# Kernel optimization log

Hardware: AMD Instinct MI355X
Metric: run time of the kernel (lower is better)

The kernel has to match this reference:

```python
import jax, jax.numpy as jnp
import numpy as np

IN_F = 2
DIM_H = 64
DT = 0.02          # step_size
INTENSITY = 40.0   # Poisson rate multiplier
RATE = jnp.array([10.0, 1.0], dtype=jnp.float32)  # Gamma rates per feature


def _xavier(key, fan_in, fan_out):
    lim = float(np.sqrt(6.0 / (fan_in + fan_out)))
    return jax.random.uniform(key, (fan_in, fan_out), minval=-lim, maxval=lim, dtype=jnp.float32)


def setup_inputs() -> dict:
    key = jax.random.key(0)
    k0, k1, k2 = jax.random.split(key, 3)
    Nsim, steps = 100000, 200
    z0 = jax.random.normal(k0, (Nsim, IN_F), dtype=jnp.float32)
    W1 = _xavier(k1, IN_F, DIM_H)
    b1 = jnp.zeros((DIM_H,), dtype=jnp.float32)
    W2 = _xavier(k2, DIM_H, IN_F)
    b2 = jnp.zeros((IN_F,), dtype=jnp.float32)
    diffusion = jnp.float32(1.0)
    return {"z0": z0, "W1": W1, "b1": b1, "W2": W2, "b2": b2,
            "diffusion": diffusion, "Nsim": Nsim, "steps": steps}


def _drift(x, W1, b1, W2, b2):
    # MLP: Linear(2,64) -> tanh -> Linear(64,2)
    h = jnp.tanh(x @ W1 + b1)
    return h @ W2 + b2


def reference(z0, W1, b1, W2, b2, diffusion, Nsim, steps):
    sqrt_dt = jnp.float32(np.sqrt(DT))
    n = z0.shape[0]

    def step(state, key):
        kp, kn, kg = jax.random.split(key, 3)
        # Poisson(intensity*dt) jump counts, shape [N,1]
        pois = jax.random.poisson(kp, INTENSITY * DT, (n, 1)).astype(jnp.float32)
        a = jnp.broadcast_to(pois, (n, IN_F))  # Gamma concentration per feature
        # Gamma(conc=pois, rate=RATE); conc==0 -> sample is exactly 0
        g = jax.random.gamma(kg, jnp.maximum(a, 1.0), dtype=jnp.float32) / RATE
        jump = jnp.where(a > 0, g, 0.0)
        noise = jax.random.normal(kn, (n, IN_F), dtype=jnp.float32)
        new_state = (state
                     + _drift(state, W1, b1, W2, b2) * DT
                     + diffusion * sqrt_dt * noise
                     + jump)
        return new_state, new_state

    keys = jax.random.split(jax.random.key(42), steps)
    _, path = jax.lax.scan(step, z0, keys)            # [steps, N, F]
    path = jnp.concatenate([z0[None], path], axis=0)   # [steps+1, N, F]
    return jnp.transpose(path, (1, 0, 2))              # [N, steps+1, F]
```

## Files before the change

kernel.cpp:

```cpp
#include <hip/hip_runtime.h>
#include <cstdint>
#include <cmath>

#define DEVINL __device__ __forceinline__

struct U2 { uint32_t a, b; };
typedef float v2f __attribute__((ext_vector_type(2)));

DEVINL uint32_t rotl32(uint32_t x, uint32_t r){ return (x << r) | (x >> (32u - r)); }

DEVINL U2 tf(uint32_t k0, uint32_t k1, uint32_t x0, uint32_t x1){
  const uint32_t k2 = k0 ^ k1 ^ 0x1BD11BDAu;
  x0 += k0; x1 += k1;
#define TFR(r) { x0 += x1; x1 = rotl32(x1,(r)); x1 ^= x0; }
  TFR(13) TFR(15) TFR(26) TFR(6)  x0 += k1; x1 += k2 + 1u;
  TFR(17) TFR(29) TFR(16) TFR(24) x0 += k2; x1 += k0 + 2u;
  TFR(13) TFR(15) TFR(26) TFR(6)  x0 += k0; x1 += k1 + 3u;
  TFR(17) TFR(29) TFR(16) TFR(24) x0 += k1; x1 += k2 + 4u;
  TFR(13) TFR(15) TFR(26) TFR(6)  x0 += k2; x1 += k0 + 5u;
#undef TFR
  U2 r; r.a = x0; r.b = x1; return r;
}

DEVINL uint32_t pbits(uint32_t k0, uint32_t k1, uint32_t idx){
  U2 r = tf(k0, k1, 0u, idx);
  return r.a ^ r.b;
}

DEVINL float u01(uint32_t bits){
  return __uint_as_float((bits >> 9) | 0x3F800000u) - 1.0f;
}

DEVINL float xla_logf(float xin){
  float xf = fmaxf(__uint_as_float(0x00800000u), xin);
  uint32_t ib = __float_as_uint(xf);
  float e = (float)((int)(ib >> 23) - 126);
  float x = __uint_as_float((ib & 0x807fffffu) | 0x3f000000u);
  bool m = x < 0.707106781186547524f;
  float t = m ? x : 0.0f;
  x = __fsub_rn(x, 1.0f);
  if (m) e = __fsub_rn(e, 1.0f);
  x = __fadd_rn(x, t);
  float z = __fmul_rn(x, x);
  float y = 7.0376836292e-2f;
  y = fmaf(y, x, -1.1514610310e-1f);
  y = fmaf(y, x,  1.1676998740e-1f);
  y = fmaf(y, x, -1.2420140846e-1f);
  y = fmaf(y, x,  1.4249322787e-1f);
  y = fmaf(y, x, -1.6668057665e-1f);
  y = fmaf(y, x,  2.0000714765e-1f);
  y = fmaf(y, x, -2.4999993993e-1f);
  y = fmaf(y, x,  3.3333331174e-1f);
  y = __fmul_rn(y, x);
  y = __fmul_rn(y, z);
  y = fmaf(e, -2.12194440e-4f, y);
  y = fmaf(z, -0.5f, y);
  x = __fadd_rn(x, y);
  x = fmaf(e, 0.693359375f, x);
  if (xin == 0.0f) x = __uint_as_float(0xff800000u);
  return x;
}

DEVINL float xla_log1pf(float v){
  float av = fabsf(v);
  if (av < 1e-4f) return __fmul_rn(__fadd_rn(__fmul_rn(-0.5f, v), 1.0f), v);
  return xla_logf(__fadd_rn(v, 1.0f));
}

DEVINL float erfinv32(float x){
  float xx = __fmul_rn(x, x);
  float w = -xla_log1pf(-xx);
  float p;
  if (w < 5.0f){
    float ww = __fsub_rn(w, 2.5f);
    p = 2.81022636e-08f;
    p = __fadd_rn( 3.43273939e-07f, __fmul_rn(p, ww));
    p = __fadd_rn(-3.5233877e-06f,  __fmul_rn(p, ww));
    p = __fadd_rn(-4.39150654e-06f, __fmul_rn(p, ww));
    p = __fadd_rn( 0.00021858087f,  __fmul_rn(p, ww));
    p = __fadd_rn(-0.00125372503f,  __fmul_rn(p, ww));
    p = __fadd_rn(-0.00417768164f,  __fmul_rn(p, ww));
    p = __fadd_rn( 0.246640727f,    __fmul_rn(p, ww));
    p = __fadd_rn( 1.50140941f,     __fmul_rn(p, ww));
  } else {
    float ww = __fsub_rn(sqrtf(w), 3.0f);
    p = -0.000200214257f;
    p = __fadd_rn( 0.000100950558f, __fmul_rn(p, ww));
    p = __fadd_rn( 0.00134934322f,  __fmul_rn(p, ww));
    p = __fadd_rn(-0.00367342844f,  __fmul_rn(p, ww));
    p = __fadd_rn( 0.00573950773f,  __fmul_rn(p, ww));
    p = __fadd_rn(-0.0076224613f,   __fmul_rn(p, ww));
    p = __fadd_rn( 0.00943887047f,  __fmul_rn(p, ww));
    p = __fadd_rn( 1.00167406f,     __fmul_rn(p, ww));
    p = __fadd_rn( 2.83297682f,     __fmul_rn(p, ww));
  }
  return __fmul_rn(p, x);
}

#define SQRT2F (__uint_as_float(0x3FB504F3u))
#define NLOF   (__uint_as_float(0xBF7FFFFFu))

DEVINL float normal_from_bits(uint32_t bits){
  float ff = u01(bits);
  float u = __fadd_rn(__fmul_rn(ff, 2.0f), NLOF);
  u = fmaxf(NLOF, u);
  return __fmul_rn(SQRT2F, erfinv32(u));
}

DEVINL float fast_tanh(float x){
  float ax = fabsf(x);
  float e = __expf(-2.0f * ax);
  float r = (1.0f - e) * __builtin_amdgcn_rcpf(1.0f + e);
  return __builtin_copysignf(r, x);
}

DEVINL v2f f2fma(v2f a, v2f b, v2f c){ return __builtin_elementwise_fma(a, b, c); }

DEVINL float gamma_one(uint32_t gk0, uint32_t gk1, float alpha){
  const float d = __fsub_rn(alpha, (1.0f/3.0f));
  const float c = (1.0f/3.0f) / sqrtf(d);
  U2 K = tf(gk0, gk1, 0u, 0u);
  for (;;) {
    U2 xk = tf(K.a, K.b, 0u, 1u);
    U2 Uk = tf(K.a, K.b, 0u, 2u);
    float xx, v;
    for (;;) {
      U2 sub = tf(xk.a, xk.b, 0u, 1u);
      uint32_t nb = pbits(sub.a, sub.b, 0u);
      xx = normal_from_bits(nb);
      v = __fadd_rn(1.0f, __fmul_rn(xx, c));
      if (v > 0.0f) break;
      xk = tf(xk.a, xk.b, 0u, 0u);
    }
    float X = __fmul_rn(xx, xx);
    float V = __fmul_rn(__fmul_rn(v, v), v);
    float U = u01(pbits(Uk.a, Uk.b, 0u));
    float sq = __fsub_rn(1.0f, __fmul_rn(0.0331f, __fmul_rn(X, X)));
    if (U < sq) return __fmul_rn(d, V);
    float lnU = xla_logf(U);
    float lnV = xla_logf(V);
    float rhs = __fadd_rn(__fmul_rn(X, 0.5f),
                          __fmul_rn(d, __fadd_rn(__fsub_rn(1.0f, V), lnV)));
    if (lnU < rhs) return __fmul_rn(d, V);
    K = tf(K.a, K.b, 0u, 0u);
  }
}

#define NPK 24
#define WSTRIDE (4 + 2*NPK)
#define KEYOFF 8
#define JOFF   16384

__global__ void setup_kernel(uint32_t* __restrict__ ws, int steps){
  int t = blockIdx.x * blockDim.x + threadIdx.x;
  if (t >= steps) return;
  U2 kt = tf(0u, 42u, 0u, (uint32_t)t);
  U2 kp = tf(kt.a, kt.b, 0u, 0u);
  U2 kn = tf(kt.a, kt.b, 0u, 1u);
  U2 kg = tf(kt.a, kt.b, 0u, 2u);
  uint32_t* p = ws + KEYOFF + (size_t)t * WSTRIDE;
  p[0] = kn.a; p[1] = kn.b;
  p[2] = kg.a; p[3] = kg.b;
  uint32_t r0 = kp.a, r1 = kp.b;
  for (int i = 0; i < NPK; ++i) {
    U2 sub = tf(r0, r1, 0u, 1u);
    U2 rn  = tf(r0, r1, 0u, 0u);
    p[4 + 2*i] = sub.a; p[5 + 2*i] = sub.b;
    r0 = rn.a; r1 = rn.b;
  }
}

__global__ __launch_bounds__(256) void pois_kernel(
    uint32_t* __restrict__ ws, int N, int steps, uint32_t POFF, uint32_t COFF)
{
  __shared__ uint32_t cnts[4];
  int e = blockIdx.x * 256 + threadIdx.x;
  int t = blockIdx.y;
  bool act = e < N;
  const uint32_t* __restrict__ p = ws + KEYOFF + (size_t)t * WSTRIDE;
  int pois = 0;
  if (act) {
    float lp = 0.0f; int k = 0;
    #pragma unroll 1
    for (int i = 0; i < NPK; ++i) {
      if (!(lp > -0.8f)) break;
      k++;
      uint32_t bits = pbits(p[4 + 2*i], p[5 + 2*i], (uint32_t)e);
      lp = __fadd_rn(lp, xla_logf(u01(bits)));
    }
    pois = k - 1;
    float* jarr = (float*)(ws + JOFF);
    size_t jb = (size_t)t * (size_t)(2*N) + 2u*(uint32_t)e;
    jarr[jb] = 0.0f; jarr[jb + 1] = 0.0f;
    ((uint8_t*)ws)[(size_t)POFF*4u + (size_t)t*(size_t)N + (size_t)e] = (uint8_t)pois;
  }
  uint64_t b = __ballot(act && (pois > 0));
  int lane = threadIdx.x & 63, w = threadIdx.x >> 6;
  if (lane == 0) cnts[w] = (uint32_t)__popcll(b);
  __syncthreads();
  if (threadIdx.x == 0)
    ws[COFF + (size_t)blockIdx.y * gridDim.x + blockIdx.x] =
        cnts[0] + cnts[1] + cnts[2] + cnts[3];
}

__global__ __launch_bounds__(256) void prefix_kernel(
    uint32_t* __restrict__ ws, uint32_t COFF, uint32_t BOFF, int NB)
{
  __shared__ uint32_t ssum[256];
  int i = threadIdx.x;
  int chunk = (NB + 255) >> 8;
  int lo = i * chunk, hi = lo + chunk; if (hi > NB) hi = NB;
  uint32_t s = 0;
  for (int j = lo; j < hi; ++j) s += ws[COFF + j];
  ssum[i] = s;
  __syncthreads();
  if (i == 0) {
    uint32_t run = 0;
    for (int k = 0; k < 256; ++k) { uint32_t c = ssum[k]; ssum[k] = run; run += c; }
    ws[0] = run;
  }
  __syncthreads();
  uint32_t base = ssum[i];
  for (int j = lo; j < hi; ++j) { ws[BOFF + j] = base; base += ws[COFF + j]; }
}

__global__ __launch_bounds__(256) void scatter_kernel(
    uint32_t* __restrict__ ws, int N, int steps,
    uint32_t POFF, uint32_t BOFF, uint32_t WOFF, uint32_t CAP)
{
  __shared__ uint32_t cnts[4];
  int e = blockIdx.x * 256 + threadIdx.x;
  int t = blockIdx.y;
  bool act = e < N;
  uint32_t pv = 0;
  if (act) pv = ((const uint8_t*)ws)[(size_t)POFF*4u + (size_t)t*(size_t)N + (size_t)e];
  uint64_t b = __ballot(pv > 0);
  int lane = threadIdx.x & 63, w = threadIdx.x >> 6;
  if (lane == 0) cnts[w] = (uint32_t)__popcll(b);
  __syncthreads();
  uint32_t bid = (uint32_t)blockIdx.y * gridDim.x + blockIdx.x;
  uint32_t wb = ws[BOFF + bid];
  for (int w2 = 0; w2 < w; ++w2) wb += cnts[w2];
  if (pv > 0) {
    uint32_t rank = (uint32_t)__popcll(b & ((1ull << lane) - 1ull));
    uint32_t idx = wb + rank;
    if (idx < CAP)
      ws[WOFF + idx] = ((uint32_t)t << 23) | ((uint32_t)e << 6) | pv;
  }
}

__global__ __launch_bounds__(256) void gamma_kernel(
    uint32_t* __restrict__ ws, int N, uint32_t WOFF, uint32_t CAP)
{
  uint32_t total = ws[0]; if (total > CAP) total = CAP;
  uint32_t j = blockIdx.x * 256u + threadIdx.x;
  if (j >= 2u * total) return;
  uint32_t ent = ws[WOFF + (j >> 1)];
  uint32_t t = ent >> 23, e = (ent >> 6) & 0x1FFFFu, pv = ent & 0x3Fu;
  const uint32_t* __restrict__ p = ws + KEYOFF + (size_t)t * WSTRIDE;
  uint32_t f = j & 1u;
  U2 gk = tf(p[2], p[3], 0u, 2u*e + f);
  float s = gamma_one(gk.a, gk.b, (float)pv);
  float* jarr = (float*)(ws + JOFF);
  jarr[(size_t)t * (size_t)(2*N) + (size_t)(2u*e + f)] = f ? s : (s / 10.0f);
}

__global__ __launch_bounds__(256) void jump_kernel(
    uint32_t* __restrict__ ws, int N, int steps)
{
  int e = blockIdx.x * 256 + threadIdx.x;
  int t = blockIdx.y;
  if (e >= N) return;
  const uint32_t* __restrict__ p = ws + KEYOFF + (size_t)t * WSTRIDE;
  const uint32_t ue = (uint32_t)e;
  float lp = 0.0f; int k = 0;
  #pragma unroll 1
  for (int i = 0; i < NPK; ++i) {
    if (!(lp > -0.8f)) break;
    k++;
    uint32_t bits = pbits(p[4 + 2*i], p[5 + 2*i], ue);
    lp = __fadd_rn(lp, xla_logf(u01(bits)));
  }
  int pois = k - 1;
  float* jarr = (float*)(ws + JOFF);
  size_t jbase = (size_t)t * (size_t)(2*N) + (size_t)(2*e);
  float j0 = 0.0f, j1 = 0.0f;
  if (pois > 0) {
    uint32_t kg0 = p[2], kg1 = p[3];
    float alpha = (float)pois;
    U2 gk0 = tf(kg0, kg1, 0u, 2u*ue);
    j0 = gamma_one(gk0.a, gk0.b, alpha) / 10.0f;
    U2 gk1 = tf(kg0, kg1, 0u, 2u*ue + 1u);
    j1 = gamma_one(gk1.a, gk1.b, alpha);
  }
  jarr[jbase] = j0; jarr[jbase + 1] = j1;
}

#define IBLK 256
__global__ __launch_bounds__(IBLK) void integrate_kernel(
    const float* __restrict__ z0, const float* __restrict__ W1,
    const float* __restrict__ b1, const float* __restrict__ W2,
    const float* __restrict__ b2, const float* __restrict__ diffp,
    const uint32_t* __restrict__ ws, float* __restrict__ out,
    int N, int steps)
{
  __shared__ float smem[322];
  for (int k = threadIdx.x; k < 322; k += IBLK) {
    float v;
    if (k < 128)      v = W1[k];
    else if (k < 192) v = b1[k - 128];
    else if (k < 320) v = W2[k - 192];
    else              v = b2[k - 320];
    smem[k] = v;
  }
  __syncthreads();
  const float* sW1 = smem;
  const float* sb1 = smem + 128;
  const float* sW2 = smem + 192;
  const float* sb2 = smem + 320;

  int tid = blockIdx.x * IBLK + threadIdx.x;
  if (tid >= 2 * N) return;
  const int e = tid >> 1;
  const int f = tid & 1;
  const uint32_t utid = (uint32_t)tid;

  float x = z0[tid];
  const size_t obase = (size_t)e * (size_t)(steps + 1) * 2u + (size_t)f;
  out[obase] = x;

  const float DTf  = 0.02f;
  const float sqdt = (float)0.14142135623730951;
  const float coef = __fmul_rn(diffp[0], sqdt);
  const int   hbase = f << 5;
  const float* __restrict__ jarr = (const float*)(ws + JOFF);

  for (int t = 0; t < steps; ++t) {
    const uint32_t* __restrict__ p = ws + KEYOFF + (size_t)t * WSTRIDE;

    float jump = jarr[(size_t)t * (size_t)(2*N) + utid];

    float nf = normal_from_bits(pbits(p[0], p[1], utid));

    float xo = __shfl_xor(x, 1, 64);
    float xf0 = (f == 0) ? x : xo;
    float xf1 = (f == 0) ? xo : x;
    v2f xv0 = (v2f){xf0, xf0};
    v2f xv1 = (v2f){xf1, xf1};
    v2f acc = (v2f){0.0f, 0.0f};
    #pragma unroll
    for (int j = 0; j < 16; ++j) {
      int h = hbase + 2*j;
      v2f w1lo = *(const v2f*)&sW1[h];
      v2f w1hi = *(const v2f*)&sW1[64 + h];
      v2f b1v  = *(const v2f*)&sb1[h];
      v2f pre  = f2fma(xv0, w1lo, f2fma(xv1, w1hi, b1v));
      float hv0 = fast_tanh(pre.x);
      float hv1 = fast_tanh(pre.y);
      v2f w2a = *(const v2f*)&sW2[2*h];
      v2f w2b = *(const v2f*)&sW2[2*h + 2];
      acc = f2fma((v2f){hv0, hv0}, w2a, acc);
      acc = f2fma((v2f){hv1, hv1}, w2b, acc);
    }
    float q0 = acc.x + __shfl_xor(acc.x, 1, 64);
    float q1 = acc.y + __shfl_xor(acc.y, 1, 64);
    float dr = sb2[f] + ((f == 0) ? q0 : q1);

    x = __fadd_rn(__fadd_rn(__fadd_rn(x, __fmul_rn(dr, DTf)),
                            __fmul_rn(coef, nf)), jump);
    out[obase + (size_t)(t + 1) * 2u] = x;
  }
}

__global__ __launch_bounds__(64) void sim_fallback_kernel(
    const float* __restrict__ z0, const float* __restrict__ W1,
    const float* __restrict__ b1, const float* __restrict__ W2,
    const float* __restrict__ b2, const float* __restrict__ diffp,
    const uint32_t* __restrict__ ws, float* __restrict__ out,
    int N, int steps)
{
  __shared__ float smem[322];
  for (int k = threadIdx.x; k < 322; k += 64) {
    float v;
    if (k < 128)      v = W1[k];
    else if (k < 192) v = b1[k - 128];
    else if (k < 320) v = W2[k - 192];
    else              v = b2[k - 320];
    smem[k] = v;
  }
  __syncthreads();
  const float* sW1 = smem;
  const float* sb1 = smem + 128;
  const float* sW2 = smem + 192;
  const float* sb2 = smem + 320;

  int tid = blockIdx.x * 64 + threadIdx.x;
  if (tid >= 2 * N) return;
  const int e = tid >> 1;
  const int f = tid & 1;
  const uint32_t ue   = (uint32_t)e;
  const uint32_t utid = (uint32_t)tid;

  float x = z0[tid];
  const size_t obase = (size_t)e * (size_t)(steps + 1) * 2u + (size_t)f;
  out[obase] = x;

  const float DTf  = 0.02f;
  const float sqdt = (float)0.14142135623730951;
  const float coef = __fmul_rn(diffp[0], sqdt);
  const int   hbase = f << 5;

  for (int t = 0; t < steps; ++t) {
    const uint32_t* __restrict__ p = ws + KEYOFF + (size_t)t * WSTRIDE;
    int pois;
    {
      float lp = 0.0f;
      pois = NPK - 1;
      #pragma unroll 1
      for (int m = 0; m < NPK/2; ++m) {
        int i0 = 2*m + f;
        uint32_t bits = pbits(p[4 + 2*i0], p[5 + 2*i0], ue);
        float lmine = xla_logf(u01(bits));
        float lother = __shfl_xor(lmine, 1, 64);
        float la = (f == 0) ? lmine : lother;
        float lb = (f == 0) ? lother : lmine;
        float s1 = __fadd_rn(lp, la);
        float s2 = __fadd_rn(s1, lb);
        if (!(s1 > -0.8f)) { pois = 2*m; break; }
        if (!(s2 > -0.8f)) { pois = 2*m + 1; break; }
        lp = s2;
      }
    }
    float nf = normal_from_bits(pbits(p[0], p[1], utid));
    float jump = 0.0f;
    if (pois > 0) {
      U2 gk = tf(p[2], p[3], 0u, utid);
      float s = gamma_one(gk.a, gk.b, (float)pois);
      jump = (f == 0) ? (s / 10.0f) : s;
    }
    float xo = __shfl_xor(x, 1, 64);
    float xf0 = (f == 0) ? x : xo;
    float xf1 = (f == 0) ? xo : x;
    float p0 = 0.0f, p1 = 0.0f;
    #pragma unroll
    for (int i = 0; i < 32; ++i) {
      int h = hbase + i;
      float hv = fast_tanh(fmaf(xf0, sW1[h], fmaf(xf1, sW1[64 + h], sb1[h])));
      p0 = fmaf(hv, sW2[2*h],     p0);
      p1 = fmaf(hv, sW2[2*h + 1], p1);
    }
    float q0 = p0 + __shfl_xor(p0, 1, 64);
    float q1 = p1 + __shfl_xor(p1, 1, 64);
    float dr = sb2[f] + ((f == 0) ? q0 : q1);
    x = __fadd_rn(__fadd_rn(__fadd_rn(x, __fmul_rn(dr, DTf)),
                            __fmul_rn(coef, nf)), jump);
    out[obase + (size_t)(t + 1) * 2u] = x;
  }
}

extern "C" void kernel_launch(void* const* d_in, const int* in_sizes, int n_in,
                              void* d_out, int out_size, void* d_ws, size_t ws_size,
                              hipStream_t stream) {
  const float* z0  = (const float*)d_in[0];
  const float* W1  = (const float*)d_in[1];
  const float* b1  = (const float*)d_in[2];
  const float* W2  = (const float*)d_in[3];
  const float* b2  = (const float*)d_in[4];
  const float* dif = (const float*)d_in[5];
  int N = in_sizes[0] / 2;
  int steps = out_size / (N * 2) - 1;
  uint32_t* ws = (uint32_t*)d_ws;
  int total = 2 * N;

  hipLaunchKernelGGL(setup_kernel, dim3((steps + 255) / 256), dim3(256), 0, stream,
                     ws, steps);

  size_t JSZ = (size_t)2 * (size_t)N * (size_t)steps;
  size_t PSZ = ((size_t)N * (size_t)steps + 3u) / 4u;
  int    NBX = (N + 255) / 256;
  size_t NB  = (size_t)NBX * (size_t)steps;
  size_t CAP = ((size_t)N * (size_t)steps * 11u) / 16u;
  size_t POFFs = (size_t)JOFF + JSZ;
  size_t COFFs = POFFs + PSZ;
  size_t BOFFs = COFFs + NB;
  size_t WOFFs = BOFFs + NB;
  size_t need0 = (WOFFs + CAP) * 4u;
  size_t need1 = ((size_t)JOFF + JSZ) * 4u;
  bool pk = (N < (1 << 17)) && (steps < (1 << 9)) && (steps <= 314) &&
            (WOFFs + CAP < 0xFFFFFFFFull);

  if (pk && ws_size >= need0) {
    hipLaunchKernelGGL(pois_kernel, dim3(NBX, steps), dim3(256), 0, stream,
                       ws, N, steps, (uint32_t)POFFs, (uint32_t)COFFs);
    hipLaunchKernelGGL(prefix_kernel, dim3(1), dim3(256), 0, stream,
                       ws, (uint32_t)COFFs, (uint32_t)BOFFs, (int)NB);
    hipLaunchKernelGGL(scatter_kernel, dim3(NBX, steps), dim3(256), 0, stream,
                       ws, N, steps, (uint32_t)POFFs, (uint32_t)BOFFs,
                       (uint32_t)WOFFs, (uint32_t)CAP);
    size_t gth = 2u * CAP;
    hipLaunchKernelGGL(gamma_kernel, dim3((gth + 255) / 256), dim3(256), 0, stream,
                       ws, N, (uint32_t)WOFFs, (uint32_t)CAP);
    hipLaunchKernelGGL(integrate_kernel, dim3((total + IBLK - 1) / IBLK), dim3(IBLK),
                       0, stream, z0, W1, b1, W2, b2, dif, ws, (float*)d_out, N, steps);
  } else if (steps <= 314 && ws_size >= need1) {
    hipLaunchKernelGGL(jump_kernel, dim3((N + 255) / 256, steps), dim3(256), 0, stream,
                       ws, N, steps);
    hipLaunchKernelGGL(integrate_kernel, dim3((total + IBLK - 1) / IBLK), dim3(IBLK),
                       0, stream, z0, W1, b1, W2, b2, dif, ws, (float*)d_out, N, steps);
  } else {
    hipLaunchKernelGGL(sim_fallback_kernel, dim3((total + 63) / 64), dim3(64), 0, stream,
                       z0, W1, b1, W2, b2, dif, ws, (float*)d_out, N, steps);
  }
}
```

Measured before the change: 1.664 ms.

## Compact Poisson sampling across elements per wave and scalarize MLP drift loop

The Poisson kernel now launches 64-thread blocks where each lane handles four elements in sequence. A lane that finishes one element's Poisson loop moves on to the next immediately, so lanes with short draws no longer sit idle waiting for the longest draw in the wave. The per-block count is reduced with a wave shuffle instead of shared memory and a syncthreads. Separately, the integrate kernel's hidden-layer loop is rewritten from packed v2f FMAs to scalar fmaf, which may change the instruction mix. The block count per step is still 256 elements, so the count layout the later kernels rely on is unchanged.

```diff
diff --git a/kernel.cpp b/kernel.cpp
--- a/kernel.cpp
+++ b/kernel.cpp
@@ -5,7 +5,6 @@
 #define DEVINL __device__ __forceinline__
 
 struct U2 { uint32_t a, b; };
-typedef float v2f __attribute__((ext_vector_type(2)));
 
 DEVINL uint32_t rotl32(uint32_t x, uint32_t r){ return (x << r) | (x >> (32u - r)); }
 
@@ -114,8 +113,6 @@
   return __builtin_copysignf(r, x);
 }
 
-DEVINL v2f f2fma(v2f a, v2f b, v2f c){ return __builtin_elementwise_fma(a, b, c); }
-
 DEVINL float gamma_one(uint32_t gk0, uint32_t gk1, float alpha){
   const float d = __fsub_rn(alpha, (1.0f/3.0f));
   const float c = (1.0f/3.0f) / sqrtf(d);
@@ -170,37 +167,63 @@
   }
 }
 
-__global__ __launch_bounds__(256) void pois_kernel(
+#define PEL 4
+__global__ __launch_bounds__(64) void pois_kernel(
     uint32_t* __restrict__ ws, int N, int steps, uint32_t POFF, uint32_t COFF)
 {
-  __shared__ uint32_t cnts[4];
-  int e = blockIdx.x * 256 + threadIdx.x;
-  int t = blockIdx.y;
-  bool act = e < N;
+  const int lane = threadIdx.x;
+  const int t = blockIdx.y;
+  const int base = blockIdx.x * (64 * PEL);
   const uint32_t* __restrict__ p = ws + KEYOFF + (size_t)t * WSTRIDE;
-  int pois = 0;
-  if (act) {
-    float lp = 0.0f; int k = 0;
-    #pragma unroll 1
-    for (int i = 0; i < NPK; ++i) {
-      if (!(lp > -0.8f)) break;
+
+  int poisv[PEL];
+  #pragma unroll
+  for (int j = 0; j < PEL; ++j) poisv[j] = -1;
+
+  int cur = 0;
+  int e = base + lane;
+  float lp = 0.0f; int k = 0;
+  bool done = (e >= N);
+
+  #pragma unroll 1
+  for (int guard = 0; guard < PEL * NPK + PEL + 1; ++guard) {
+    if (!__any(!done)) break;
+    if (!done) {
+      if (!(lp > -0.8f)) {
+        poisv[cur] = k - 1;
+        cur++;
+        lp = 0.0f; k = 0;
+        int ne = base + cur * 64 + lane;
+        if (cur >= PEL || ne >= N) done = true;
+        else e = ne;
+      }
+    }
+    if (!done) {
+      uint32_t bits = pbits(p[4 + 2*k], p[5 + 2*k], (uint32_t)e);
+      lp = __fadd_rn(lp, xla_logf(u01(bits)));
       k++;
-      uint32_t bits = pbits(p[4 + 2*i], p[5 + 2*i], (uint32_t)e);
-      lp = __fadd_rn(lp, xla_logf(u01(bits)));
-    }
-    pois = k - 1;
-    float* jarr = (float*)(ws + JOFF);
-    size_t jb = (size_t)t * (size_t)(2*N) + 2u*(uint32_t)e;
-    jarr[jb] = 0.0f; jarr[jb + 1] = 0.0f;
-    ((uint8_t*)ws)[(size_t)POFF*4u + (size_t)t*(size_t)N + (size_t)e] = (uint8_t)pois;
-  }
-  uint64_t b = __ballot(act && (pois > 0));
-  int lane = threadIdx.x & 63, w = threadIdx.x >> 6;
-  if (lane == 0) cnts[w] = (uint32_t)__popcll(b);
-  __syncthreads();
-  if (threadIdx.x == 0)
-    ws[COFF + (size_t)blockIdx.y * gridDim.x + blockIdx.x] =
-        cnts[0] + cnts[1] + cnts[2] + cnts[3];
+      if (k >= NPK) lp = -1.0f;
+    }
+  }
+
+  float* jarr = (float*)(ws + JOFF);
+  uint8_t* pb = (uint8_t*)ws + (size_t)POFF * 4u + (size_t)t * (size_t)N;
+  int mycnt = 0;
+  #pragma unroll
+  for (int j = 0; j < PEL; ++j) {
+    int ej = base + j * 64 + lane;
+    if (ej < N) {
+      pb[ej] = (uint8_t)poisv[j];
+      size_t jb = (size_t)t * (size_t)(2*N) + 2u * (uint32_t)ej;
+      jarr[jb] = 0.0f; jarr[jb + 1] = 0.0f;
+      if (poisv[j] > 0) mycnt++;
+    }
+  }
+  int c = mycnt;
+  #pragma unroll
+  for (int off = 32; off > 0; off >>= 1) c += __shfl_xor(c, off, 64);
+  if (lane == 0)
+    ws[COFF + (size_t)t * gridDim.x + blockIdx.x] = (uint32_t)c;
 }
 
 __global__ __launch_bounds__(256) void prefix_kernel(
@@ -345,25 +368,16 @@
     float xo = __shfl_xor(x, 1, 64);
     float xf0 = (f == 0) ? x : xo;
     float xf1 = (f == 0) ? xo : x;
-    v2f xv0 = (v2f){xf0, xf0};
-    v2f xv1 = (v2f){xf1, xf1};
-    v2f acc = (v2f){0.0f, 0.0f};
+    float p0 = 0.0f, p1 = 0.0f;
     #pragma unroll
-    for (int j = 0; j < 16; ++j) {
-      int h = hbase + 2*j;
-      v2f w1lo = *(const v2f*)&sW1[h];
-      v2f w1hi = *(const v2f*)&sW1[64 + h];
-      v2f b1v  = *(const v2f*)&sb1[h];
-      v2f pre  = f2fma(xv0, w1lo, f2fma(xv1, w1hi, b1v));
-      float hv0 = fast_tanh(pre.x);
-      float hv1 = fast_tanh(pre.y);
-      v2f w2a = *(const v2f*)&sW2[2*h];
-      v2f w2b = *(const v2f*)&sW2[2*h + 2];
-      acc = f2fma((v2f){hv0, hv0}, w2a, acc);
-      acc = f2fma((v2f){hv1, hv1}, w2b, acc);
-    }
-    float q0 = acc.x + __shfl_xor(acc.x, 1, 64);
-    float q1 = acc.y + __shfl_xor(acc.y, 1, 64);
+    for (int i = 0; i < 32; ++i) {
+      int h = hbase + i;
+      float hv = fast_tanh(fmaf(xf0, sW1[h], fmaf(xf1, sW1[64 + h], sb1[h])));
+      p0 = fmaf(hv, sW2[2*h],     p0);
+      p1 = fmaf(hv, sW2[2*h + 1], p1);
+    }
+    float q0 = p0 + __shfl_xor(p0, 1, 64);
+    float q1 = p1 + __shfl_xor(p1, 1, 64);
     float dr = sb2[f] + ((f == 0) ? q0 : q1);
 
     x = __fadd_rn(__fadd_rn(__fadd_rn(x, __fmul_rn(dr, DTf)),
@@ -490,7 +504,7 @@
             (WOFFs + CAP < 0xFFFFFFFFull);
 
   if (pk && ws_size >= need0) {
-    hipLaunchKernelGGL(pois_kernel, dim3(NBX, steps), dim3(256), 0, stream,
+    hipLaunchKernelGGL(pois_kernel, dim3(NBX, steps), dim3(64), 0, stream,
                        ws, N, steps, (uint32_t)POFFs, (uint32_t)COFFs);
     hipLaunchKernelGGL(prefix_kernel, dim3(1), dim3(256), 0, stream,
                        ws, (uint32_t)COFFs, (uint32_t)BOFFs, (int)NB);
```

Measured after the change: 1.729 ms. 1.04x slower.
